# Kernel tuning notes

Measured on AMD Instinct MI355X. Metric: run time of the kernel, lower is better.

Reference implementation:

```python
import jax, jax.numpy as jnp
import numpy as np

NUM_RBF = 16
MAX_REL = 32          # max_relative_feature
AUTOREGRESSIVE = True
D_MIN, D_MAX = 2.0, 22.0
LN_EPS = 1e-5


def setup_inputs() -> dict:
    key = jax.random.key(0)
    ks = jax.random.split(key, 6)
    B, L, A, K = 1, 1280, 14, 30
    E_feat, edge_in = 128, 16 + NUM_RBF * 4 * 10  # 656
    X = jax.random.normal(ks[0], (B, L, A, 3), dtype=jnp.float32) * 3.0
    residue_idx = jnp.tile(jnp.arange(L, dtype=jnp.int32)[None], (B, 1))
    chain_labels = jnp.zeros((B, L), dtype=jnp.int32)
    E_idx = jax.random.randint(ks[1], (B, L, K), 0, L, dtype=jnp.int32)
    atom_mask = jnp.ones((B, L, A), dtype=jnp.float32)
    W_pos = jax.random.normal(ks[2], (2 * MAX_REL + 2, 16), dtype=jnp.float32) * 0.1
    b_pos = jnp.zeros((16,), dtype=jnp.float32)
    W_edge = jax.random.normal(ks[3], (edge_in, E_feat), dtype=jnp.float32) * 0.05
    ln_gamma = jnp.ones((E_feat,), dtype=jnp.float32)
    ln_beta = jnp.zeros((E_feat,), dtype=jnp.float32)
    return {"X": X, "residue_idx": residue_idx, "chain_labels": chain_labels,
            "E_idx": E_idx, "atom_mask": atom_mask, "W_pos": W_pos,
            "b_pos": b_pos, "W_edge": W_edge, "ln_gamma": ln_gamma,
            "ln_beta": ln_beta}


def _forward(X, residue_idx, chain_labels, E_idx, W_pos, b_pos, W_edge,
             ln_gamma, ln_beta):
    B, L, A, _ = X.shape
    K = E_idx.shape[-1]
    # backbone atoms in loop order [Ca, N, C, O] -> X indices [1, 0, 2, 3]
    bb = X[:, :, jnp.array([1, 0, 2, 3]), :]          # [B, L, 4, 3]
    sc = X[:, :, 4:, :]                               # [B, L, 10, 3]
    Abb = jnp.transpose(bb, (0, 2, 1, 3))             # [B, 4, L, 3]
    Asc = jnp.transpose(sc, (0, 2, 1, 3))             # [B, 10, L, 3]
    # dense pairwise distances for all 40 (bb, sc) atom pairs: [B,4,10,L,L]
    diff = Abb[:, :, None, :, None, :] - Asc[:, None, :, None, :, :]
    D = jnp.sqrt(jnp.sum(diff * diff, axis=-1) + 1e-6)
    # gather top-k neighbor columns -> [B,4,10,L,K]
    D_nb = jnp.take_along_axis(D, E_idx[:, None, None, :, :], axis=4)
    mu = jnp.linspace(D_MIN, D_MAX, NUM_RBF, dtype=D_nb.dtype)
    sigma = (D_MAX - D_MIN) / NUM_RBF
    RBF = jnp.exp(-(((D_nb[..., None] - mu) / sigma) ** 2))  # [B,4,10,L,K,16]
    if AUTOREGRESSIVE:
        self_edges = (E_idx == jnp.arange(L, dtype=E_idx.dtype)[None, :, None])
        RBF = jnp.where(self_edges[:, None, None, :, :, None], 0.0, RBF)
    # concat order: bb outer, sc inner -> [B,L,K, 4*10*16]
    RBF_all = jnp.transpose(RBF, (0, 3, 4, 1, 2, 5)).reshape(B, L, K, 4 * 10 * NUM_RBF)
    # positional encodings
    offset = residue_idx[:, :, None] - residue_idx[:, None, :]        # [B,L,L]
    offset = jnp.take_along_axis(offset, E_idx, axis=2)               # [B,L,K]
    d_chains = (chain_labels[:, :, None] == chain_labels[:, None, :]).astype(jnp.int32)
    E_chains = jnp.take_along_axis(d_chains, E_idx, axis=2)           # [B,L,K]
    d = jnp.clip(offset + MAX_REL, 0, 2 * MAX_REL) * E_chains + (1 - E_chains) * (2 * MAX_REL + 1)
    d_onehot = jax.nn.one_hot(d, 2 * MAX_REL + 2, dtype=W_pos.dtype)  # [B,L,K,66]
    E_positional = d_onehot @ W_pos + b_pos                           # [B,L,K,16]
    E = jnp.concatenate([E_positional, RBF_all], axis=-1)             # [B,L,K,656]
    E = E @ W_edge                                                    # no bias
    # LayerNorm over last dim
    mean = jnp.mean(E, axis=-1, keepdims=True)
    var = jnp.mean((E - mean) ** 2, axis=-1, keepdims=True)
    E = (E - mean) / jnp.sqrt(var + LN_EPS) * ln_gamma + ln_beta
    return E


def reference(X, residue_idx, chain_labels, E_idx, atom_mask, W_pos, b_pos,
              W_edge, ln_gamma, ln_beta):
    E = _forward(X, residue_idx, chain_labels, E_idx, W_pos, b_pos, W_edge,
                 ln_gamma, ln_beta)
    return (E, E_idx)
```

## Files before the change

kernel.cpp:

```cpp
#include <hip/hip_runtime.h>

typedef short    bf16x8 __attribute__((ext_vector_type(8)));
typedef float    f32x4  __attribute__((ext_vector_type(4)));
typedef unsigned u32x4  __attribute__((ext_vector_type(4)));

#define L_RES 1280
#define A_ATM 14
#define K_NB  30
#define FEAT  656
#define NKB   21
#define NCH   128
#define FRAG  512
#define E_OUT_OFF (L_RES * K_NB * NCH)

__device__ __forceinline__ ushort f2bf(float x) {
    union { float f; unsigned u; } v; v.f = x;
    unsigned r = (v.u + 0x7fffu + ((v.u >> 16) & 1u)) >> 16;
    return (ushort)r;
}
__device__ __forceinline__ unsigned pkbf(float lo, float hi) {
    union { float f; unsigned u; } a, b; a.f = lo; b.f = hi;
    return (a.u >> 16) | (b.u & 0xffff0000u);
}

__global__ __launch_bounds__(256) void prep_kernel(const float* __restrict__ W,
                                                   ushort* __restrict__ Wpack) {
    int u = blockIdx.x * 256 + threadIdx.x;
    if (u >= 84 * 128) return;
    int kbq = u >> 7, n = u & 127;
    int kb = kbq >> 2, quad = kbq & 3;
    ushort val[8];
#pragma unroll
    for (int j = 0; j < 8; j++) {
        int k = kb * 32 + quad * 8 + j;
        val[j] = (k < FEAT) ? f2bf(W[k * NCH + n]) : (ushort)0;
    }
    ushort* dst = Wpack + (size_t)((((n >> 4) * NKB + kb) * 64 + quad * 16 + (n & 15)) * 8);
    *(ulonglong2*)dst = *(const ulonglong2*)val;
}

__global__ __launch_bounds__(256) void sidechain_fused_kernel(
    const float* __restrict__ X,
    const int*   __restrict__ ridx,
    const int*   __restrict__ clab,
    const int*   __restrict__ Eidx,
    const float* __restrict__ Wpos,
    const float* __restrict__ bpos,
    const ushort* __restrict__ Wpack,
    const float* __restrict__ gamma,
    const float* __restrict__ beta,
    float* __restrict__ out)
{
    __shared__ __align__(16) float scj[2][K_NB][10][4];
    __shared__ float bbs[2][4][3];
    __shared__ __align__(16) float xch[2][16][64][4];

    const int blk  = blockIdx.x;
    const int t    = threadIdx.x;
    const int w    = t >> 6;
    const int lane = t & 63;
    const int rh   = w & 1;
    const int kh   = w >> 1;
    const int i    = blk * 2 + rh;
    const int frow = lane & 15;
    const int quad = lane >> 4;

    if (t < 24) {
        const int perm[4] = {1, 0, 2, 3};
        int r = t / 12, rr = t - r * 12, a = rr / 3, c = rr - a * 3;
        bbs[r][a][c] = X[((blk * 2 + r) * A_ATM + perm[a]) * 3 + c];
    }
#pragma unroll
    for (int idx = t; idx < 600; idx += 256) {
        int r = idx / 300, rem = idx - r * 300;
        int e = rem / 10, a = rem - e * 10;
        int j = Eidx[(blk * 2 + r) * K_NB + e];
        const float* xp = X + ((size_t)j * A_ATM + 4 + a) * 3;
        float4 v = make_float4(xp[0], xp[1], xp[2], 0.f);
        *(float4*)&scj[r][e][a][0] = v;
    }
    __syncthreads();

    const int e0 = frow, e1 = 16 + frow;
    const bool v1 = (e1 < K_NB);
    const int j0 = Eidx[i * K_NB + e0];
    const int j1 = v1 ? Eidx[i * K_NB + e1] : 0;
    const bool ok0 = (j0 != i);
    const bool ok1 = v1 && (j1 != i);
    int d0 = 65, d1 = 65;
    {
        int ci = clab[i], ri = ridx[i];
        if (ci == clab[j0]) { int o = ri - ridx[j0] + 32; d0 = o < 0 ? 0 : (o > 64 ? 64 : o); }
        if (ci == clab[j1]) { int o = ri - ridx[j1] + 32; d1 = o < 0 ? 0 : (o > 64 ? 64 : o); }
    }

    const int kb_lo = kh ? 11 : 0;
    const int kb_hi = kh ? NKB : 11;
    const ushort* Bbase = Wpack + (size_t)lane * 8;

    f32x4 acc0[8], acc1[8];
#pragma unroll
    for (int n = 0; n < 8; n++) {
        acc0[n] = (f32x4){0.f, 0.f, 0.f, 0.f};
        acc1[n] = (f32x4){0.f, 0.f, 0.f, 0.f};
    }

    const float cs = 0.96089795f;
    const float mustep = 1.33333333f * cs;
    const int   r0 = (quad & 1) * 8;
    const float mubase = (2.0f + (float)r0 * 1.33333333f) * cs;

    for (int kb = kb_lo; kb < kb_hi; kb++) {
        bf16x8 b[8];
#pragma unroll
        for (int n = 0; n < 8; n++)
            b[n] = *(const bf16x8*)(Bbase + (size_t)(n * NKB + kb) * FRAG);

        union { u32x4 u; bf16x8 h; } A0, A1;
        if (kb == 0 && quad < 2) {
            float p0[8], p1[8];
#pragma unroll
            for (int j = 0; j < 8; j++) {
                int c = quad * 8 + j;
                float bp = bpos[c];
                p0[j] = Wpos[d0 * 16 + c] + bp;
                p1[j] = v1 ? (Wpos[d1 * 16 + c] + bp) : 0.f;
            }
#pragma unroll
            for (int jj = 0; jj < 4; jj++) {
                A0.u[jj] = pkbf(p0[2 * jj], p0[2 * jj + 1]);
                A1.u[jj] = pkbf(p1[2 * jj], p1[2 * jj + 1]);
            }
        } else {
            bool kv = !(kb == NKB - 1 && quad >= 2);
            int p  = kv ? (2 * kb - 1 + (quad >> 1)) : 0;
            int ab = p / 10, as = p - ab * 10;
            float bx = bbs[rh][ab][0], by = bbs[rh][ab][1], bz = bbs[rh][ab][2];
            f32x4 s0 = *(const f32x4*)&scj[rh][e0][as][0];
            f32x4 s1 = *(const f32x4*)&scj[rh][v1 ? e1 : 0][as][0];
            float dx0 = bx - s0[0], dy0 = by - s0[1], dz0 = bz - s0[2];
            float dx1 = bx - s1[0], dy1 = by - s1[1], dz1 = bz - s1[2];
            float dd0 = sqrtf(dx0 * dx0 + dy0 * dy0 + dz0 * dz0 + 1e-6f) * cs - mubase;
            float dd1 = sqrtf(dx1 * dx1 + dy1 * dy1 + dz1 * dz1 + 1e-6f) * cs - mubase;
            bool m0 = kv && ok0, m1 = kv && ok1;
#pragma unroll
            for (int jj = 0; jj < 4; jj++) {
                float cA = (float)(2 * jj) * mustep;
                float cB = (float)(2 * jj + 1) * mustep;
                float tA0 = dd0 - cA, tB0 = dd0 - cB;
                float tA1 = dd1 - cA, tB1 = dd1 - cB;
                unsigned q0 = pkbf(exp2f(-(tA0 * tA0)), exp2f(-(tB0 * tB0)));
                unsigned q1 = pkbf(exp2f(-(tA1 * tA1)), exp2f(-(tB1 * tB1)));
                A0.u[jj] = m0 ? q0 : 0u;
                A1.u[jj] = m1 ? q1 : 0u;
            }
        }
#pragma unroll
        for (int n = 0; n < 8; n++)
            acc0[n] = __builtin_amdgcn_mfma_f32_16x16x32_bf16(A0.h, b[n], acc0[n], 0, 0, 0);
#pragma unroll
        for (int n = 0; n < 8; n++)
            acc1[n] = __builtin_amdgcn_mfma_f32_16x16x32_bf16(A1.h, b[n], acc1[n], 0, 0, 0);
    }

    if (kh == 1) {
#pragma unroll
        for (int n = 0; n < 8; n++) {
            *(f32x4*)&xch[rh][n][lane][0]     = acc0[n];
            *(f32x4*)&xch[rh][8 + n][lane][0] = acc1[n];
        }
        if (lane < K_NB) out[E_OUT_OFF + i * K_NB + lane] = (float)Eidx[i * K_NB + lane];
    }
    __syncthreads();
    if (kh == 0) {
#pragma unroll
        for (int n = 0; n < 8; n++) {
            acc0[n] += *(const f32x4*)&xch[rh][n][lane][0];
            acc1[n] += *(const f32x4*)&xch[rh][8 + n][lane][0];
        }
        float g[8], bt[8];
#pragma unroll
        for (int n = 0; n < 8; n++) {
            g[n]  = gamma[n * 16 + frow];
            bt[n] = beta[n * 16 + frow];
        }
#pragma unroll
        for (int m = 0; m < 2; m++) {
            f32x4* acc = m ? acc1 : acc0;
#pragma unroll
            for (int r = 0; r < 4; r++) {
                float s = 0.f, q = 0.f;
#pragma unroll
                for (int n = 0; n < 8; n++) {
                    float v = acc[n][r];
                    s += v; q += v * v;
                }
#pragma unroll
                for (int off = 1; off < 16; off <<= 1) {
                    s += __shfl_xor(s, off);
                    q += __shfl_xor(q, off);
                }
                float mean = s * (1.0f / 128.0f);
                float var  = q * (1.0f / 128.0f) - mean * mean;
                float rstd = rsqrtf(var + 1e-5f);
                int edge = m * 16 + quad * 4 + r;
                if (edge < K_NB) {
                    float* o = out + ((size_t)i * K_NB + edge) * NCH + frow;
#pragma unroll
                    for (int n = 0; n < 8; n++)
                        o[n * 16] = (acc[n][r] - mean) * rstd * g[n] + bt[n];
                }
            }
        }
    }
}

extern "C" void kernel_launch(void* const* d_in, const int* in_sizes, int n_in,
                              void* d_out, int out_size, void* d_ws, size_t ws_size,
                              hipStream_t stream) {
    const float* X     = (const float*)d_in[0];
    const int*   ridx  = (const int*)  d_in[1];
    const int*   clab  = (const int*)  d_in[2];
    const int*   Eidx  = (const int*)  d_in[3];
    const float* Wpos  = (const float*)d_in[5];
    const float* bpos  = (const float*)d_in[6];
    const float* Wedge = (const float*)d_in[7];
    const float* gamma = (const float*)d_in[8];
    const float* beta  = (const float*)d_in[9];
    float* out = (float*)d_out;

    ushort* Wpack = (ushort*)d_ws;

    prep_kernel<<<42, 256, 0, stream>>>(Wedge, Wpack);
    sidechain_fused_kernel<<<L_RES / 2, 256, 0, stream>>>(
        X, ridx, clab, Eidx, Wpos, bpos, Wpack, gamma, beta, out);
}
```

Before: 110.1 us.

## Fuse weight packing into main kernel with double-buffered LDS slabs

```diff
diff --git a/kernel.cpp b/kernel.cpp
--- a/kernel.cpp
+++ b/kernel.cpp
@@ -10,207 +10,185 @@
 #define FEAT  656
 #define NKB   21
 #define NCH   128
-#define FRAG  512
+#define SLAB_K 40
 #define E_OUT_OFF (L_RES * K_NB * NCH)
 
 __device__ __forceinline__ ushort f2bf(float x) {
     union { float f; unsigned u; } v; v.f = x;
-    unsigned r = (v.u + 0x7fffu + ((v.u >> 16) & 1u)) >> 16;
-    return (ushort)r;
+    return (ushort)((v.u + 0x7fffu + ((v.u >> 16) & 1u)) >> 16);
+}
+__device__ __forceinline__ unsigned pk2rne(float lo, float hi) {
+    return (unsigned)f2bf(lo) | ((unsigned)f2bf(hi) << 16);
 }
 __device__ __forceinline__ unsigned pkbf(float lo, float hi) {
     union { float f; unsigned u; } a, b; a.f = lo; b.f = hi;
     return (a.u >> 16) | (b.u & 0xffff0000u);
 }
 
-__global__ __launch_bounds__(256) void prep_kernel(const float* __restrict__ W,
-                                                   ushort* __restrict__ Wpack) {
-    int u = blockIdx.x * 256 + threadIdx.x;
-    if (u >= 84 * 128) return;
-    int kbq = u >> 7, n = u & 127;
-    int kb = kbq >> 2, quad = kbq & 3;
-    ushort val[8];
-#pragma unroll
-    for (int j = 0; j < 8; j++) {
-        int k = kb * 32 + quad * 8 + j;
-        val[j] = (k < FEAT) ? f2bf(W[k * NCH + n]) : (ushort)0;
-    }
-    ushort* dst = Wpack + (size_t)((((n >> 4) * NKB + kb) * 64 + quad * 16 + (n & 15)) * 8);
-    *(ulonglong2*)dst = *(const ulonglong2*)val;
-}
-
-__global__ __launch_bounds__(256) void sidechain_fused_kernel(
+__global__ __launch_bounds__(256) void sidechain_one_kernel(
     const float* __restrict__ X,
     const int*   __restrict__ ridx,
     const int*   __restrict__ clab,
     const int*   __restrict__ Eidx,
     const float* __restrict__ Wpos,
     const float* __restrict__ bpos,
-    const ushort* __restrict__ Wpack,
+    const float* __restrict__ Wedge,
     const float* __restrict__ gamma,
     const float* __restrict__ beta,
     float* __restrict__ out)
 {
+    __shared__ ushort slab[2][NCH][SLAB_K];
     __shared__ __align__(16) float scj[2][K_NB][10][4];
     __shared__ float bbs[2][4][3];
-    __shared__ __align__(16) float xch[2][16][64][4];
 
     const int blk  = blockIdx.x;
     const int t    = threadIdx.x;
     const int w    = t >> 6;
     const int lane = t & 63;
     const int rh   = w & 1;
-    const int kh   = w >> 1;
+    const int mt   = w >> 1;
     const int i    = blk * 2 + rh;
     const int frow = lane & 15;
     const int quad = lane >> 4;
+
+    auto stage_slab = [&](int kb, int p) {
+        unsigned* base = (unsigned*)&slab[p][0][0];
+#pragma unroll
+        for (int s = 0; s < 2; s++) {
+            int g  = s * 256 + t;
+            int kp = g & 15, cq = g >> 4;
+            int k  = kb * 32 + 2 * kp;
+            if (k + 1 < FEAT) {
+                const float* src = Wedge + (size_t)k * NCH + cq * 4;
+                float4 r0 = *(const float4*)src;
+                float4 r1 = *(const float4*)(src + NCH);
+                base[(4 * cq + 0) * (SLAB_K / 2) + kp] = pk2rne(r0.x, r1.x);
+                base[(4 * cq + 1) * (SLAB_K / 2) + kp] = pk2rne(r0.y, r1.y);
+                base[(4 * cq + 2) * (SLAB_K / 2) + kp] = pk2rne(r0.z, r1.z);
+                base[(4 * cq + 3) * (SLAB_K / 2) + kp] = pk2rne(r0.w, r1.w);
+            } else {
+                base[(4 * cq + 0) * (SLAB_K / 2) + kp] = 0u;
+                base[(4 * cq + 1) * (SLAB_K / 2) + kp] = 0u;
+                base[(4 * cq + 2) * (SLAB_K / 2) + kp] = 0u;
+                base[(4 * cq + 3) * (SLAB_K / 2) + kp] = 0u;
+            }
+        }
+    };
 
     if (t < 24) {
         const int perm[4] = {1, 0, 2, 3};
         int r = t / 12, rr = t - r * 12, a = rr / 3, c = rr - a * 3;
         bbs[r][a][c] = X[((blk * 2 + r) * A_ATM + perm[a]) * 3 + c];
     }
-#pragma unroll
+    if (t < 2 * K_NB) {
+        int gid = blk * 2 * K_NB + t;
+        out[E_OUT_OFF + gid] = (float)Eidx[gid];
+    }
     for (int idx = t; idx < 600; idx += 256) {
         int r = idx / 300, rem = idx - r * 300;
         int e = rem / 10, a = rem - e * 10;
         int j = Eidx[(blk * 2 + r) * K_NB + e];
         const float* xp = X + ((size_t)j * A_ATM + 4 + a) * 3;
-        float4 v = make_float4(xp[0], xp[1], xp[2], 0.f);
-        *(float4*)&scj[r][e][a][0] = v;
-    }
+        *(float4*)&scj[r][e][a][0] = make_float4(xp[0], xp[1], xp[2], 0.f);
+    }
+    stage_slab(0, 0);
+
+    const int  eA = mt * 16 + frow;
+    const bool vA = (eA < K_NB);
+    const int  jA = vA ? Eidx[i * K_NB + eA] : 0;
+    const bool okA = vA && (jA != i);
+    int dA = 65;
+    if (vA && clab[i] == clab[jA]) {
+        int o = ridx[i] - ridx[jA] + 32;
+        dA = o < 0 ? 0 : (o > 64 ? 64 : o);
+    }
+
+    const float cs     = 0.96089795f;
+    const float mustep = 1.33333333f * cs;
+    const int   r0     = (quad & 1) * 8;
+    const float mubase = (2.0f + (float)r0 * 1.33333333f) * cs;
+
+    f32x4 acc[8];
+#pragma unroll
+    for (int n = 0; n < 8; n++) acc[n] = (f32x4){0.f, 0.f, 0.f, 0.f};
+
     __syncthreads();
 
-    const int e0 = frow, e1 = 16 + frow;
-    const bool v1 = (e1 < K_NB);
-    const int j0 = Eidx[i * K_NB + e0];
-    const int j1 = v1 ? Eidx[i * K_NB + e1] : 0;
-    const bool ok0 = (j0 != i);
-    const bool ok1 = v1 && (j1 != i);
-    int d0 = 65, d1 = 65;
-    {
-        int ci = clab[i], ri = ridx[i];
-        if (ci == clab[j0]) { int o = ri - ridx[j0] + 32; d0 = o < 0 ? 0 : (o > 64 ? 64 : o); }
-        if (ci == clab[j1]) { int o = ri - ridx[j1] + 32; d1 = o < 0 ? 0 : (o > 64 ? 64 : o); }
-    }
-
-    const int kb_lo = kh ? 11 : 0;
-    const int kb_hi = kh ? NKB : 11;
-    const ushort* Bbase = Wpack + (size_t)lane * 8;
-
-    f32x4 acc0[8], acc1[8];
-#pragma unroll
-    for (int n = 0; n < 8; n++) {
-        acc0[n] = (f32x4){0.f, 0.f, 0.f, 0.f};
-        acc1[n] = (f32x4){0.f, 0.f, 0.f, 0.f};
-    }
-
-    const float cs = 0.96089795f;
-    const float mustep = 1.33333333f * cs;
-    const int   r0 = (quad & 1) * 8;
-    const float mubase = (2.0f + (float)r0 * 1.33333333f) * cs;
-
-    for (int kb = kb_lo; kb < kb_hi; kb++) {
-        bf16x8 b[8];
+    for (int kb = 0; kb < NKB; kb++) {
+        if (kb + 1 < NKB) stage_slab(kb + 1, (kb + 1) & 1);
+
+        const int p = kb & 1;
+        bf16x8 bfr[8];
 #pragma unroll
         for (int n = 0; n < 8; n++)
-            b[n] = *(const bf16x8*)(Bbase + (size_t)(n * NKB + kb) * FRAG);
-
-        union { u32x4 u; bf16x8 h; } A0, A1;
+            bfr[n] = *(const bf16x8*)&slab[p][n * 16 + frow][quad * 8];
+
+        union { u32x4 u; bf16x8 h; } A;
         if (kb == 0 && quad < 2) {
-            float p0[8], p1[8];
+            float pv[8];
 #pragma unroll
             for (int j = 0; j < 8; j++) {
                 int c = quad * 8 + j;
-                float bp = bpos[c];
-                p0[j] = Wpos[d0 * 16 + c] + bp;
-                p1[j] = v1 ? (Wpos[d1 * 16 + c] + bp) : 0.f;
+                pv[j] = vA ? (Wpos[dA * 16 + c] + bpos[c]) : 0.f;
             }
 #pragma unroll
-            for (int jj = 0; jj < 4; jj++) {
-                A0.u[jj] = pkbf(p0[2 * jj], p0[2 * jj + 1]);
-                A1.u[jj] = pkbf(p1[2 * jj], p1[2 * jj + 1]);
-            }
+            for (int jj = 0; jj < 4; jj++)
+                A.u[jj] = pkbf(pv[2 * jj], pv[2 * jj + 1]);
         } else {
-            bool kv = !(kb == NKB - 1 && quad >= 2);
-            int p  = kv ? (2 * kb - 1 + (quad >> 1)) : 0;
-            int ab = p / 10, as = p - ab * 10;
+            int  pr = 2 * kb - 1 + (quad >> 1);
+            bool kv = (pr < 40);
+            int  pp = kv ? pr : 0;
+            int  ab = pp / 10, as = pp - ab * 10;
             float bx = bbs[rh][ab][0], by = bbs[rh][ab][1], bz = bbs[rh][ab][2];
-            f32x4 s0 = *(const f32x4*)&scj[rh][e0][as][0];
-            f32x4 s1 = *(const f32x4*)&scj[rh][v1 ? e1 : 0][as][0];
-            float dx0 = bx - s0[0], dy0 = by - s0[1], dz0 = bz - s0[2];
-            float dx1 = bx - s1[0], dy1 = by - s1[1], dz1 = bz - s1[2];
-            float dd0 = sqrtf(dx0 * dx0 + dy0 * dy0 + dz0 * dz0 + 1e-6f) * cs - mubase;
-            float dd1 = sqrtf(dx1 * dx1 + dy1 * dy1 + dz1 * dz1 + 1e-6f) * cs - mubase;
-            bool m0 = kv && ok0, m1 = kv && ok1;
+            f32x4 sc = *(const f32x4*)&scj[rh][vA ? eA : 0][as][0];
+            float dx = bx - sc[0], dy = by - sc[1], dz = bz - sc[2];
+            float dd = sqrtf(dx * dx + dy * dy + dz * dz + 1e-6f) * cs - mubase;
+            bool m = kv && okA;
 #pragma unroll
             for (int jj = 0; jj < 4; jj++) {
                 float cA = (float)(2 * jj) * mustep;
                 float cB = (float)(2 * jj + 1) * mustep;
-                float tA0 = dd0 - cA, tB0 = dd0 - cB;
-                float tA1 = dd1 - cA, tB1 = dd1 - cB;
-                unsigned q0 = pkbf(exp2f(-(tA0 * tA0)), exp2f(-(tB0 * tB0)));
-                unsigned q1 = pkbf(exp2f(-(tA1 * tA1)), exp2f(-(tB1 * tB1)));
-                A0.u[jj] = m0 ? q0 : 0u;
-                A1.u[jj] = m1 ? q1 : 0u;
+                float tA = dd - cA, tB = dd - cB;
+                unsigned q = pkbf(exp2f(-(tA * tA)), exp2f(-(tB * tB)));
+                A.u[jj] = m ? q : 0u;
             }
         }
+
 #pragma unroll
         for (int n = 0; n < 8; n++)
-            acc0[n] = __builtin_amdgcn_mfma_f32_16x16x32_bf16(A0.h, b[n], acc0[n], 0, 0, 0);
-#pragma unroll
-        for (int n = 0; n < 8; n++)
-            acc1[n] = __builtin_amdgcn_mfma_f32_16x16x32_bf16(A1.h, b[n], acc1[n], 0, 0, 0);
-    }
-
-    if (kh == 1) {
+            acc[n] = __builtin_amdgcn_mfma_f32_16x16x32_bf16(A.h, bfr[n], acc[n], 0, 0, 0);
+
+        __syncthreads();
+    }
+
+    float g[8], bt[8];
+#pragma unroll
+    for (int n = 0; n < 8; n++) {
+        g[n]  = gamma[n * 16 + frow];
+        bt[n] = beta[n * 16 + frow];
+    }
+#pragma unroll
+    for (int r = 0; r < 4; r++) {
+        float s = 0.f, q = 0.f;
 #pragma unroll
         for (int n = 0; n < 8; n++) {
-            *(f32x4*)&xch[rh][n][lane][0]     = acc0[n];
-            *(f32x4*)&xch[rh][8 + n][lane][0] = acc1[n];
-        }
-        if (lane < K_NB) out[E_OUT_OFF + i * K_NB + lane] = (float)Eidx[i * K_NB + lane];
-    }
-    __syncthreads();
-    if (kh == 0) {
-#pragma unroll
-        for (int n = 0; n < 8; n++) {
-            acc0[n] += *(const f32x4*)&xch[rh][n][lane][0];
-            acc1[n] += *(const f32x4*)&xch[rh][8 + n][lane][0];
-        }
-        float g[8], bt[8];
-#pragma unroll
-        for (int n = 0; n < 8; n++) {
-            g[n]  = gamma[n * 16 + frow];
-            bt[n] = beta[n * 16 + frow];
-        }
-#pragma unroll
-        for (int m = 0; m < 2; m++) {
-            f32x4* acc = m ? acc1 : acc0;
-#pragma unroll
-            for (int r = 0; r < 4; r++) {
-                float s = 0.f, q = 0.f;
-#pragma unroll
-                for (int n = 0; n < 8; n++) {
-                    float v = acc[n][r];
-                    s += v; q += v * v;
-                }
-#pragma unroll
-                for (int off = 1; off < 16; off <<= 1) {
-                    s += __shfl_xor(s, off);
-                    q += __shfl_xor(q, off);
-                }
-                float mean = s * (1.0f / 128.0f);
-                float var  = q * (1.0f / 128.0f) - mean * mean;
-                float rstd = rsqrtf(var + 1e-5f);
-                int edge = m * 16 + quad * 4 + r;
-                if (edge < K_NB) {
-                    float* o = out + ((size_t)i * K_NB + edge) * NCH + frow;
-#pragma unroll
-                    for (int n = 0; n < 8; n++)
-                        o[n * 16] = (acc[n][r] - mean) * rstd * g[n] + bt[n];
-                }
-            }
+            float v = acc[n][r];
+            s += v; q += v * v;
+        }
+#pragma unroll
+        for (int off = 1; off < 16; off <<= 1) {
+            s += __shfl_xor(s, off);
+            q += __shfl_xor(q, off);
+        }
+        float mean = s * (1.0f / 128.0f);
+        float var  = q * (1.0f / 128.0f) - mean * mean;
+        float rstd = rsqrtf(var + 1e-5f);
+        int edge = mt * 16 + quad * 4 + r;
+        if (edge < K_NB) {
+            float* o = out + ((size_t)i * K_NB + edge) * NCH + frow;
+#pragma unroll
+            for (int n = 0; n < 8; n++)
+                o[n * 16] = (acc[n][r] - mean) * rstd * g[n] + bt[n];
         }
     }
 }
@@ -229,9 +207,6 @@
     const float* beta  = (const float*)d_in[9];
     float* out = (float*)d_out;
 
-    ushort* Wpack = (ushort*)d_ws;
-
-    prep_kernel<<<42, 256, 0, stream>>>(Wedge, Wpack);
-    sidechain_fused_kernel<<<L_RES / 2, 256, 0, stream>>>(
-        X, ridx, clab, Eidx, Wpos, bpos, Wpack, gamma, beta, out);
-}
+    sidechain_one_kernel<<<L_RES / 2, 256, 0, stream>>>(
+        X, ridx, clab, Eidx, Wpos, bpos, Wedge, gamma, beta, out);
+}
```

New measurement: 117.4 us. 6.6% more time.
